# Kernel optimization log

Measured on AMD Instinct MI355X. Metric: run time of the kernel, lower is better.

Reference implementation:

```python
import jax, jax.numpy as jnp
import numpy as np

B, N, H = 32, 2048, 512
MASK_NEG = 1e30  # matches torch mask_logic constant


def setup_inputs() -> dict:
    key = jax.random.key(0)
    ks = jax.random.split(key, 10)
    Q = jax.random.normal(ks[0], (B, H), dtype=jnp.float32)
    K = jax.random.normal(ks[1], (B, N, H), dtype=jnp.float32)
    V = jax.random.normal(ks[2], (B, N, H), dtype=jnp.float32)
    adj = jax.random.randint(ks[3], (B, N), 0, 2, dtype=jnp.int32)
    s_mask = jax.random.randint(ks[4], (B, N), 0, 2, dtype=jnp.int32)
    s = 1.0 / np.sqrt(H)
    w_att = jax.random.uniform(ks[5], (1, 2 * H), jnp.float32, -s, s)  # nn.Linear(2H,1) weight
    b_att = jax.random.uniform(ks[6], (1,), jnp.float32, -s, s)
    Wr0 = jax.random.uniform(ks[7], (H, H), jnp.float32, -s, s)
    Wr1 = jax.random.uniform(ks[8], (H, H), jnp.float32, -s, s)
    Wri = jax.random.uniform(ks[9], (H, H), jnp.float32, -s, s)
    return {"Q": Q, "K": K, "V": V, "adj": adj, "s_mask": s_mask,
            "w_att": w_att, "b_att": b_att, "Wr0": Wr0, "Wr1": Wr1, "Wri": Wri}


def reference(Q, K, V, adj, s_mask, w_att, b_att, Wr0, Wr1, Wri):
    Hdim = Q.shape[-1]
    # additive score: linear(cat(Q_exp, K)) split into Q-part + K-part (avoids materializing [B,N,2H])
    wq, wk = w_att[:, :Hdim], w_att[:, Hdim:]          # [1,H] each
    alpha = (Q @ wq[0]) [:, None] + K @ wk[0] + b_att[0]  # [B,N]
    # adjacency mask + softmax over neighbors
    masked = alpha - (1.0 - adj.astype(jnp.float32)) * MASK_NEG
    attn = jax.nn.softmax(masked, axis=1)               # [B,N]
    # gated value projection: V0 where s_mask==1, V1 where 0
    V0 = jnp.einsum('bnh,oh->bno', V, Wr0)
    V1 = jnp.einsum('bnh,oh->bno', V, Wr1)
    sm = s_mask.astype(jnp.float32)[..., None]          # [B,N,1]
    Vm = V0 * sm + V1 * (1.0 - sm)
    # weighted aggregation + residual projection
    attn_sum = jnp.einsum('bn,bnh->bh', attn, Vm) + Q @ Wri.T
    return attn[:, None, :], attn_sum                   # ([B,1,N], [B,H])
```

## Files before the change

kernel.cpp:

```cpp
#include <hip/hip_runtime.h>

#define BB 32
#define NN 2048
#define HH 512
#define MASK_NEG 1e30f

static __device__ __forceinline__ float dot4(float4 a, float4 b) {
    return a.x * b.x + a.y * b.y + a.z * b.z + a.w * b.w;
}

__global__ void k_scores(const float* __restrict__ K,
                         const float* __restrict__ w_att,
                         const int* __restrict__ adj,
                         float* __restrict__ scores) {
    int wave = (blockIdx.x * blockDim.x + threadIdx.x) >> 6;
    int lane = threadIdx.x & 63;
    if (wave >= BB * NN) return;
    const float* wk = w_att + HH;
    size_t base = (size_t)wave * HH;
    float4 k0 = *(const float4*)(K + base + lane * 4);
    float4 k1 = *(const float4*)(K + base + 256 + lane * 4);
    float4 a0 = *(const float4*)(wk + lane * 4);
    float4 a1 = *(const float4*)(wk + 256 + lane * 4);
    float s = dot4(k0, a0) + dot4(k1, a1);
#pragma unroll
    for (int off = 32; off > 0; off >>= 1) s += __shfl_down(s, off, 64);
    if (lane == 0) scores[wave] = adj[wave] ? s : -MASK_NEG;
}

__global__ void k_softmax(float* __restrict__ attn) {
    __shared__ float red[4];
    int b = blockIdx.x;
    int t = threadIdx.x;
    float v[8];
    float m = -INFINITY;
#pragma unroll
    for (int i = 0; i < 8; i++) {
        v[i] = attn[b * NN + t * 8 + i];
        m = fmaxf(m, v[i]);
    }
#pragma unroll
    for (int off = 32; off > 0; off >>= 1) m = fmaxf(m, __shfl_xor(m, off, 64));
    if ((t & 63) == 0) red[t >> 6] = m;
    __syncthreads();
    float m4 = fmaxf(fmaxf(red[0], red[1]), fmaxf(red[2], red[3]));
    float sum = 0.0f;
#pragma unroll
    for (int i = 0; i < 8; i++) {
        v[i] = expf(v[i] - m4);
        sum += v[i];
    }
#pragma unroll
    for (int off = 32; off > 0; off >>= 1) sum += __shfl_xor(sum, off, 64);
    __syncthreads();
    if ((t & 63) == 0) red[t >> 6] = sum;
    __syncthreads();
    float inv = 1.0f / (red[0] + red[1] + red[2] + red[3]);
#pragma unroll
    for (int i = 0; i < 8; i++) attn[b * NN + t * 8 + i] = v[i] * inv;
}

__global__ void k_wsum(const float* __restrict__ V,
                       const float* __restrict__ attn,
                       const int* __restrict__ s_mask,
                       float* __restrict__ u0,
                       float* __restrict__ u1) {
    int b = blockIdx.x >> 4;
    int chunk = blockIdx.x & 15;
    int n0 = chunk * 128;
    int t = threadIdx.x;
    int h4 = (t & 127) * 4;
    int half = t >> 7;
    __shared__ float w0s[128], w1s[128];
    if (t < 128) {
        float w = attn[b * NN + n0 + t];
        int sm = s_mask[b * NN + n0 + t];
        w0s[t] = sm ? w : 0.0f;
        w1s[t] = sm ? 0.0f : w;
    }
    __syncthreads();
    float4 a0 = {0, 0, 0, 0}, a1 = {0, 0, 0, 0};
    const float* Vb = V + ((size_t)(b * NN + n0 + half * 64)) * HH + h4;
#pragma unroll 4
    for (int i = 0; i < 64; i++) {
        float4 x = *(const float4*)(Vb + (size_t)i * HH);
        float w0 = w0s[half * 64 + i];
        float w1 = w1s[half * 64 + i];
        a0.x += w0 * x.x; a0.y += w0 * x.y; a0.z += w0 * x.z; a0.w += w0 * x.w;
        a1.x += w1 * x.x; a1.y += w1 * x.y; a1.z += w1 * x.z; a1.w += w1 * x.w;
    }
    float* p0 = u0 + b * HH + h4;
    float* p1 = u1 + b * HH + h4;
    atomicAdd(p0 + 0, a0.x); atomicAdd(p0 + 1, a0.y);
    atomicAdd(p0 + 2, a0.z); atomicAdd(p0 + 3, a0.w);
    atomicAdd(p1 + 0, a1.x); atomicAdd(p1 + 1, a1.y);
    atomicAdd(p1 + 2, a1.z); atomicAdd(p1 + 3, a1.w);
}

__global__ void k_out(const float* __restrict__ Q,
                      const float* __restrict__ Wr0,
                      const float* __restrict__ Wr1,
                      const float* __restrict__ Wri,
                      const float* __restrict__ u0,
                      const float* __restrict__ u1,
                      float* __restrict__ out) {
    int wave = (blockIdx.x * blockDim.x + threadIdx.x) >> 6;
    int lane = threadIdx.x & 63;
    if (wave >= BB * HH) return;
    int b = wave >> 9;
    int o = wave & 511;
    const float* q = Q + b * HH;
    const float* a = u0 + b * HH;
    const float* c = u1 + b * HH;
    const float* r0 = Wr0 + (size_t)o * HH;
    const float* r1 = Wr1 + (size_t)o * HH;
    const float* ri = Wri + (size_t)o * HH;
    float s = 0.0f;
#pragma unroll
    for (int part = 0; part < 2; part++) {
        int h = part * 256 + lane * 4;
        s += dot4(*(const float4*)(r0 + h), *(const float4*)(a + h));
        s += dot4(*(const float4*)(r1 + h), *(const float4*)(c + h));
        s += dot4(*(const float4*)(ri + h), *(const float4*)(q + h));
    }
#pragma unroll
    for (int off = 32; off > 0; off >>= 1) s += __shfl_down(s, off, 64);
    if (lane == 0) out[wave] = s;
}

extern "C" void kernel_launch(void* const* d_in, const int* in_sizes, int n_in,
                              void* d_out, int out_size, void* d_ws, size_t ws_size,
                              hipStream_t stream) {
    const float* Q = (const float*)d_in[0];
    const float* K = (const float*)d_in[1];
    const float* V = (const float*)d_in[2];
    const int* adj = (const int*)d_in[3];
    const int* s_mask = (const int*)d_in[4];
    const float* w_att = (const float*)d_in[5];
    const float* Wr0 = (const float*)d_in[7];
    const float* Wr1 = (const float*)d_in[8];
    const float* Wri = (const float*)d_in[9];

    float* out = (float*)d_out;
    float* attn = out;
    float* attn_sum = out + BB * NN;
    float* u0 = (float*)d_ws;
    float* u1 = u0 + BB * HH;

    hipMemsetAsync(d_ws, 0, 2 * BB * HH * sizeof(float), stream);
    k_scores<<<(BB * NN) / 4, 256, 0, stream>>>(K, w_att, adj, attn);
    k_softmax<<<BB, 256, 0, stream>>>(attn);
    k_wsum<<<BB * 16, 256, 0, stream>>>(V, attn, s_mask, u0, u1);
    k_out<<<(BB * HH) / 4, 256, 0, stream>>>(Q, Wr0, Wr1, Wri, u0, u1, attn_sum);
}
```

Baseline: 312.1 us.

## Fuse all stages into one cooperative kernel with grid-wide syncs

Replaces the memset plus four kernel launches with a single cooperative kernel of 512 blocks that zeroes the workspace, then computes scores, softmax, the masked weighted sum of V and the output projection, separated by grid.sync. Each wave now handles 32 score rows and 8 output units. The two halves of a block are combined in shared memory before the atomics, which halves atomic traffic. This removes launch gaps and per-kernel tails, but the softmax phase runs on only 32 blocks while the rest wait, and each grid sync adds latency.

```diff
diff --git a/kernel.cpp b/kernel.cpp
--- a/kernel.cpp
+++ b/kernel.cpp
@@ -1,131 +1,162 @@
 #include <hip/hip_runtime.h>
+#include <hip/hip_cooperative_groups.h>
+
+namespace cg = cooperative_groups;
 
 #define BB 32
 #define NN 2048
 #define HH 512
-#define MASK_NEG 1e30f
 
 static __device__ __forceinline__ float dot4(float4 a, float4 b) {
     return a.x * b.x + a.y * b.y + a.z * b.z + a.w * b.w;
 }
 
-__global__ void k_scores(const float* __restrict__ K,
-                         const float* __restrict__ w_att,
-                         const int* __restrict__ adj,
-                         float* __restrict__ scores) {
-    int wave = (blockIdx.x * blockDim.x + threadIdx.x) >> 6;
-    int lane = threadIdx.x & 63;
-    if (wave >= BB * NN) return;
-    const float* wk = w_att + HH;
-    size_t base = (size_t)wave * HH;
-    float4 k0 = *(const float4*)(K + base + lane * 4);
-    float4 k1 = *(const float4*)(K + base + 256 + lane * 4);
-    float4 a0 = *(const float4*)(wk + lane * 4);
-    float4 a1 = *(const float4*)(wk + 256 + lane * 4);
-    float s = dot4(k0, a0) + dot4(k1, a1);
+static __device__ __forceinline__ float waveRedSum(float s) {
 #pragma unroll
     for (int off = 32; off > 0; off >>= 1) s += __shfl_down(s, off, 64);
-    if (lane == 0) scores[wave] = adj[wave] ? s : -MASK_NEG;
+    return s;
 }
 
-__global__ void k_softmax(float* __restrict__ attn) {
-    __shared__ float red[4];
-    int b = blockIdx.x;
+__global__ void __launch_bounds__(256, 2)
+k_fused(const float* __restrict__ Q, const float* __restrict__ K,
+        const float* __restrict__ V, const int* __restrict__ adj,
+        const int* __restrict__ s_mask, const float* __restrict__ w_att,
+        const float* __restrict__ Wr0, const float* __restrict__ Wr1,
+        const float* __restrict__ Wri, float* __restrict__ out,
+        float* __restrict__ ws) {
+    cg::grid_group grid = cg::this_grid();
+    float* attn = out;
+    float* attn_sum = out + BB * NN;
+    float* u0 = ws;
+    float* u1 = ws + BB * HH;
+
+    __shared__ float smem[1280];
+
     int t = threadIdx.x;
-    float v[8];
-    float m = -INFINITY;
+    int blk = blockIdx.x;
+    int gtid = blk * 256 + t;
+    int wave = gtid >> 6;
+    int lane = t & 63;
+
+    if (gtid < 2 * BB * HH) ws[gtid] = 0.0f;
+
+    {
+        const float* wk = w_att + HH;
+        float4 a0 = *(const float4*)(wk + lane * 4);
+        float4 a1 = *(const float4*)(wk + 256 + lane * 4);
+#pragma unroll 4
+        for (int i = 0; i < 32; i++) {
+            int r = wave * 32 + i;
+            size_t base = (size_t)r * HH;
+            float4 k0 = *(const float4*)(K + base + lane * 4);
+            float4 k1 = *(const float4*)(K + base + 256 + lane * 4);
+            float s = waveRedSum(dot4(k0, a0) + dot4(k1, a1));
+            if (lane == 0) attn[r] = adj[r] ? s : -1e30f;
+        }
+    }
+    grid.sync();
+
+    if (blk < BB) {
+        float* red = smem;
+        int b = blk;
+        float v[8];
+        float m = -INFINITY;
 #pragma unroll
-    for (int i = 0; i < 8; i++) {
-        v[i] = attn[b * NN + t * 8 + i];
-        m = fmaxf(m, v[i]);
+        for (int i = 0; i < 8; i++) {
+            v[i] = attn[b * NN + t * 8 + i];
+            m = fmaxf(m, v[i]);
+        }
+#pragma unroll
+        for (int off = 32; off > 0; off >>= 1) m = fmaxf(m, __shfl_xor(m, off, 64));
+        if (lane == 0) red[t >> 6] = m;
+        __syncthreads();
+        float m4 = fmaxf(fmaxf(red[0], red[1]), fmaxf(red[2], red[3]));
+        float sum = 0.0f;
+#pragma unroll
+        for (int i = 0; i < 8; i++) {
+            v[i] = expf(v[i] - m4);
+            sum += v[i];
+        }
+#pragma unroll
+        for (int off = 32; off > 0; off >>= 1) sum += __shfl_xor(sum, off, 64);
+        __syncthreads();
+        if (lane == 0) red[t >> 6] = sum;
+        __syncthreads();
+        float inv = 1.0f / (red[0] + red[1] + red[2] + red[3]);
+#pragma unroll
+        for (int i = 0; i < 8; i++) attn[b * NN + t * 8 + i] = v[i] * inv;
     }
+    grid.sync();
+
+    {
+        float* w0s = smem;
+        float* w1s = smem + 128;
+        float* comb = smem + 256;
+        int b = blk >> 4;
+        int n0 = (blk & 15) * 128;
+        int h4 = (t & 127) * 4;
+        int half = t >> 7;
+        if (t < 128) {
+            float w = attn[b * NN + n0 + t];
+            int sm = s_mask[b * NN + n0 + t];
+            w0s[t] = sm ? w : 0.0f;
+            w1s[t] = sm ? 0.0f : w;
+        }
+        __syncthreads();
+        float4 a0 = {0, 0, 0, 0}, a1 = {0, 0, 0, 0};
+        const float* Vb = V + ((size_t)(b * NN + n0 + half * 64)) * HH + h4;
+#pragma unroll 4
+        for (int i = 0; i < 64; i++) {
+            float4 x = *(const float4*)(Vb + (size_t)i * HH);
+            float w0 = w0s[half * 64 + i];
+            float w1 = w1s[half * 64 + i];
+            a0.x += w0 * x.x; a0.y += w0 * x.y; a0.z += w0 * x.z; a0.w += w0 * x.w;
+            a1.x += w1 * x.x; a1.y += w1 * x.y; a1.z += w1 * x.z; a1.w += w1 * x.w;
+        }
+        if (half == 1) {
+            int i8 = (t - 128) * 8;
+            comb[i8 + 0] = a0.x; comb[i8 + 1] = a0.y; comb[i8 + 2] = a0.z; comb[i8 + 3] = a0.w;
+            comb[i8 + 4] = a1.x; comb[i8 + 5] = a1.y; comb[i8 + 6] = a1.z; comb[i8 + 7] = a1.w;
+        }
+        __syncthreads();
+        if (half == 0) {
+            int i8 = t * 8;
+            a0.x += comb[i8 + 0]; a0.y += comb[i8 + 1]; a0.z += comb[i8 + 2]; a0.w += comb[i8 + 3];
+            a1.x += comb[i8 + 4]; a1.y += comb[i8 + 5]; a1.z += comb[i8 + 6]; a1.w += comb[i8 + 7];
+            float* p0 = u0 + b * HH + h4;
+            float* p1 = u1 + b * HH + h4;
+            atomicAdd(p0 + 0, a0.x); atomicAdd(p0 + 1, a0.y);
+            atomicAdd(p0 + 2, a0.z); atomicAdd(p0 + 3, a0.w);
+            atomicAdd(p1 + 0, a1.x); atomicAdd(p1 + 1, a1.y);
+            atomicAdd(p1 + 2, a1.z); atomicAdd(p1 + 3, a1.w);
+        }
+    }
+    grid.sync();
+
+    {
 #pragma unroll
-    for (int off = 32; off > 0; off >>= 1) m = fmaxf(m, __shfl_xor(m, off, 64));
-    if ((t & 63) == 0) red[t >> 6] = m;
-    __syncthreads();
-    float m4 = fmaxf(fmaxf(red[0], red[1]), fmaxf(red[2], red[3]));
-    float sum = 0.0f;
+        for (int i = 0; i < 8; i++) {
+            int unit = wave * 8 + i;
+            int b = unit >> 9;
+            int o = unit & 511;
+            const float* q = Q + b * HH;
+            const float* x0 = u0 + b * HH;
+            const float* x1 = u1 + b * HH;
+            const float* r0 = Wr0 + (size_t)o * HH;
+            const float* r1 = Wr1 + (size_t)o * HH;
+            const float* ri = Wri + (size_t)o * HH;
+            float s = 0.0f;
 #pragma unroll
-    for (int i = 0; i < 8; i++) {
-        v[i] = expf(v[i] - m4);
-        sum += v[i];
+            for (int part = 0; part < 2; part++) {
+                int h = part * 256 + lane * 4;
+                s += dot4(*(const float4*)(r0 + h), *(const float4*)(x0 + h));
+                s += dot4(*(const float4*)(r1 + h), *(const float4*)(x1 + h));
+                s += dot4(*(const float4*)(ri + h), *(const float4*)(q + h));
+            }
+            s = waveRedSum(s);
+            if (lane == 0) attn_sum[unit] = s;
+        }
     }
-#pragma unroll
-    for (int off = 32; off > 0; off >>= 1) sum += __shfl_xor(sum, off, 64);
-    __syncthreads();
-    if ((t & 63) == 0) red[t >> 6] = sum;
-    __syncthreads();
-    float inv = 1.0f / (red[0] + red[1] + red[2] + red[3]);
-#pragma unroll
-    for (int i = 0; i < 8; i++) attn[b * NN + t * 8 + i] = v[i] * inv;
-}
-
-__global__ void k_wsum(const float* __restrict__ V,
-                       const float* __restrict__ attn,
-                       const int* __restrict__ s_mask,
-                       float* __restrict__ u0,
-                       float* __restrict__ u1) {
-    int b = blockIdx.x >> 4;
-    int chunk = blockIdx.x & 15;
-    int n0 = chunk * 128;
-    int t = threadIdx.x;
-    int h4 = (t & 127) * 4;
-    int half = t >> 7;
-    __shared__ float w0s[128], w1s[128];
-    if (t < 128) {
-        float w = attn[b * NN + n0 + t];
-        int sm = s_mask[b * NN + n0 + t];
-        w0s[t] = sm ? w : 0.0f;
-        w1s[t] = sm ? 0.0f : w;
-    }
-    __syncthreads();
-    float4 a0 = {0, 0, 0, 0}, a1 = {0, 0, 0, 0};
-    const float* Vb = V + ((size_t)(b * NN + n0 + half * 64)) * HH + h4;
-#pragma unroll 4
-    for (int i = 0; i < 64; i++) {
-        float4 x = *(const float4*)(Vb + (size_t)i * HH);
-        float w0 = w0s[half * 64 + i];
-        float w1 = w1s[half * 64 + i];
-        a0.x += w0 * x.x; a0.y += w0 * x.y; a0.z += w0 * x.z; a0.w += w0 * x.w;
-        a1.x += w1 * x.x; a1.y += w1 * x.y; a1.z += w1 * x.z; a1.w += w1 * x.w;
-    }
-    float* p0 = u0 + b * HH + h4;
-    float* p1 = u1 + b * HH + h4;
-    atomicAdd(p0 + 0, a0.x); atomicAdd(p0 + 1, a0.y);
-    atomicAdd(p0 + 2, a0.z); atomicAdd(p0 + 3, a0.w);
-    atomicAdd(p1 + 0, a1.x); atomicAdd(p1 + 1, a1.y);
-    atomicAdd(p1 + 2, a1.z); atomicAdd(p1 + 3, a1.w);
-}
-
-__global__ void k_out(const float* __restrict__ Q,
-                      const float* __restrict__ Wr0,
-                      const float* __restrict__ Wr1,
-                      const float* __restrict__ Wri,
-                      const float* __restrict__ u0,
-                      const float* __restrict__ u1,
-                      float* __restrict__ out) {
-    int wave = (blockIdx.x * blockDim.x + threadIdx.x) >> 6;
-    int lane = threadIdx.x & 63;
-    if (wave >= BB * HH) return;
-    int b = wave >> 9;
-    int o = wave & 511;
-    const float* q = Q + b * HH;
-    const float* a = u0 + b * HH;
-    const float* c = u1 + b * HH;
-    const float* r0 = Wr0 + (size_t)o * HH;
-    const float* r1 = Wr1 + (size_t)o * HH;
-    const float* ri = Wri + (size_t)o * HH;
-    float s = 0.0f;
-#pragma unroll
-    for (int part = 0; part < 2; part++) {
-        int h = part * 256 + lane * 4;
-        s += dot4(*(const float4*)(r0 + h), *(const float4*)(a + h));
-        s += dot4(*(const float4*)(r1 + h), *(const float4*)(c + h));
-        s += dot4(*(const float4*)(ri + h), *(const float4*)(q + h));
-    }
-#pragma unroll
-    for (int off = 32; off > 0; off >>= 1) s += __shfl_down(s, off, 64);
-    if (lane == 0) out[wave] = s;
 }
 
 extern "C" void kernel_launch(void* const* d_in, const int* in_sizes, int n_in,
@@ -140,16 +171,9 @@
     const float* Wr0 = (const float*)d_in[7];
     const float* Wr1 = (const float*)d_in[8];
     const float* Wri = (const float*)d_in[9];
+    float* out = (float*)d_out;
+    float* ws = (float*)d_ws;
 
-    float* out = (float*)d_out;
-    float* attn = out;
-    float* attn_sum = out + BB * NN;
-    float* u0 = (float*)d_ws;
-    float* u1 = u0 + BB * HH;
-
-    hipMemsetAsync(d_ws, 0, 2 * BB * HH * sizeof(float), stream);
-    k_scores<<<(BB * NN) / 4, 256, 0, stream>>>(K, w_att, adj, attn);
-    k_softmax<<<BB, 256, 0, stream>>>(attn);
-    k_wsum<<<BB * 16, 256, 0, stream>>>(V, attn, s_mask, u0, u1);
-    k_out<<<(BB * HH) / 4, 256, 0, stream>>>(Q, Wr0, Wr1, Wri, u0, u1, attn_sum);
+    void* args[] = {&Q, &K, &V, &adj, &s_mask, &w_att, &Wr0, &Wr1, &Wri, &out, &ws};
+    hipLaunchCooperativeKernel((void*)k_fused, dim3(512), dim3(256), args, 0, stream);
 }
```

After: 510.1 us. +63.4%, slower.

## Fold memset into score kernel, defer softmax normalization, combine halves before atomics

Applied to the files above, without the earlier changes.

Zeroing of the accumulation workspace moves into the score kernel, which removes the separate memset launch. The softmax kernel now only computes per-row max and inverse sum, and the weighted-sum kernel applies exp and normalization while writing the attention output, so the normalized probabilities no longer take an extra read-write pass. Inside the weighted-sum kernel the two half-blocks are summed through shared memory before the atomic adds, which halves global atomic traffic at the cost of an extra barrier and 4KB of shared memory.

```diff
diff --git a/kernel.cpp b/kernel.cpp
--- a/kernel.cpp
+++ b/kernel.cpp
@@ -3,17 +3,20 @@
 #define BB 32
 #define NN 2048
 #define HH 512
-#define MASK_NEG 1e30f
 
 static __device__ __forceinline__ float dot4(float4 a, float4 b) {
     return a.x * b.x + a.y * b.y + a.z * b.z + a.w * b.w;
 }
 
+
 __global__ void k_scores(const float* __restrict__ K,
                          const float* __restrict__ w_att,
                          const int* __restrict__ adj,
-                         float* __restrict__ scores) {
-    int wave = (blockIdx.x * blockDim.x + threadIdx.x) >> 6;
+                         float* __restrict__ scores,
+                         float* __restrict__ ws) {
+    int gtid = blockIdx.x * blockDim.x + threadIdx.x;
+    if (gtid < 2 * BB * HH) ws[gtid] = 0.0f;
+    int wave = gtid >> 6;
     int lane = threadIdx.x & 63;
     if (wave >= BB * NN) return;
     const float* wk = w_att + HH;
@@ -25,10 +28,11 @@
     float s = dot4(k0, a0) + dot4(k1, a1);
 #pragma unroll
     for (int off = 32; off > 0; off >>= 1) s += __shfl_down(s, off, 64);
-    if (lane == 0) scores[wave] = adj[wave] ? s : -MASK_NEG;
+    if (lane == 0) scores[wave] = adj[wave] ? s : -1e30f;
 }
 
-__global__ void k_softmax(float* __restrict__ attn) {
+__global__ void k_rowstats(const float* __restrict__ scores,
+                           float* __restrict__ stats) {
     __shared__ float red[4];
     int b = blockIdx.x;
     int t = threadIdx.x;
@@ -36,7 +40,7 @@
     float m = -INFINITY;
 #pragma unroll
     for (int i = 0; i < 8; i++) {
-        v[i] = attn[b * NN + t * 8 + i];
+        v[i] = scores[b * NN + t * 8 + i];
         m = fmaxf(m, v[i]);
     }
 #pragma unroll
@@ -46,34 +50,35 @@
     float m4 = fmaxf(fmaxf(red[0], red[1]), fmaxf(red[2], red[3]));
     float sum = 0.0f;
 #pragma unroll
-    for (int i = 0; i < 8; i++) {
-        v[i] = expf(v[i] - m4);
-        sum += v[i];
-    }
+    for (int i = 0; i < 8; i++) sum += expf(v[i] - m4);
 #pragma unroll
     for (int off = 32; off > 0; off >>= 1) sum += __shfl_xor(sum, off, 64);
     __syncthreads();
     if ((t & 63) == 0) red[t >> 6] = sum;
     __syncthreads();
-    float inv = 1.0f / (red[0] + red[1] + red[2] + red[3]);
-#pragma unroll
-    for (int i = 0; i < 8; i++) attn[b * NN + t * 8 + i] = v[i] * inv;
+    if (t == 0) {
+        stats[b] = m4;
+        stats[32 + b] = 1.0f / (red[0] + red[1] + red[2] + red[3]);
+    }
 }
 
 __global__ void k_wsum(const float* __restrict__ V,
-                       const float* __restrict__ attn,
+                       float* __restrict__ attn,
                        const int* __restrict__ s_mask,
+                       const float* __restrict__ stats,
                        float* __restrict__ u0,
                        float* __restrict__ u1) {
     int b = blockIdx.x >> 4;
-    int chunk = blockIdx.x & 15;
-    int n0 = chunk * 128;
+    int n0 = (blockIdx.x & 15) * 128;
     int t = threadIdx.x;
     int h4 = (t & 127) * 4;
     int half = t >> 7;
-    __shared__ float w0s[128], w1s[128];
+    __shared__ float w0s[128], w1s[128], comb[1024];
     if (t < 128) {
-        float w = attn[b * NN + n0 + t];
+        float mb = stats[b];
+        float invb = stats[32 + b];
+        float w = expf(attn[b * NN + n0 + t] - mb) * invb;
+        attn[b * NN + n0 + t] = w;
         int sm = s_mask[b * NN + n0 + t];
         w0s[t] = sm ? w : 0.0f;
         w1s[t] = sm ? 0.0f : w;
@@ -89,12 +94,23 @@
         a0.x += w0 * x.x; a0.y += w0 * x.y; a0.z += w0 * x.z; a0.w += w0 * x.w;
         a1.x += w1 * x.x; a1.y += w1 * x.y; a1.z += w1 * x.z; a1.w += w1 * x.w;
     }
-    float* p0 = u0 + b * HH + h4;
-    float* p1 = u1 + b * HH + h4;
-    atomicAdd(p0 + 0, a0.x); atomicAdd(p0 + 1, a0.y);
-    atomicAdd(p0 + 2, a0.z); atomicAdd(p0 + 3, a0.w);
-    atomicAdd(p1 + 0, a1.x); atomicAdd(p1 + 1, a1.y);
-    atomicAdd(p1 + 2, a1.z); atomicAdd(p1 + 3, a1.w);
+    if (half == 1) {
+        int i8 = (t - 128) * 8;
+        comb[i8 + 0] = a0.x; comb[i8 + 1] = a0.y; comb[i8 + 2] = a0.z; comb[i8 + 3] = a0.w;
+        comb[i8 + 4] = a1.x; comb[i8 + 5] = a1.y; comb[i8 + 6] = a1.z; comb[i8 + 7] = a1.w;
+    }
+    __syncthreads();
+    if (half == 0) {
+        int i8 = t * 8;
+        a0.x += comb[i8 + 0]; a0.y += comb[i8 + 1]; a0.z += comb[i8 + 2]; a0.w += comb[i8 + 3];
+        a1.x += comb[i8 + 4]; a1.y += comb[i8 + 5]; a1.z += comb[i8 + 6]; a1.w += comb[i8 + 7];
+        float* p0 = u0 + b * HH + h4;
+        float* p1 = u1 + b * HH + h4;
+        atomicAdd(p0 + 0, a0.x); atomicAdd(p0 + 1, a0.y);
+        atomicAdd(p0 + 2, a0.z); atomicAdd(p0 + 3, a0.w);
+        atomicAdd(p1 + 0, a1.x); atomicAdd(p1 + 1, a1.y);
+        atomicAdd(p1 + 2, a1.z); atomicAdd(p1 + 3, a1.w);
+    }
 }
 
 __global__ void k_out(const float* __restrict__ Q,
@@ -110,8 +126,8 @@
     int b = wave >> 9;
     int o = wave & 511;
     const float* q = Q + b * HH;
-    const float* a = u0 + b * HH;
-    const float* c = u1 + b * HH;
+    const float* x0 = u0 + b * HH;
+    const float* x1 = u1 + b * HH;
     const float* r0 = Wr0 + (size_t)o * HH;
     const float* r1 = Wr1 + (size_t)o * HH;
     const float* ri = Wri + (size_t)o * HH;
@@ -119,8 +135,8 @@
 #pragma unroll
     for (int part = 0; part < 2; part++) {
         int h = part * 256 + lane * 4;
-        s += dot4(*(const float4*)(r0 + h), *(const float4*)(a + h));
-        s += dot4(*(const float4*)(r1 + h), *(const float4*)(c + h));
+        s += dot4(*(const float4*)(r0 + h), *(const float4*)(x0 + h));
+        s += dot4(*(const float4*)(r1 + h), *(const float4*)(x1 + h));
         s += dot4(*(const float4*)(ri + h), *(const float4*)(q + h));
     }
 #pragma unroll
@@ -144,12 +160,13 @@
     float* out = (float*)d_out;
     float* attn = out;
     float* attn_sum = out + BB * NN;
-    float* u0 = (float*)d_ws;
-    float* u1 = u0 + BB * HH;
+    float* ws = (float*)d_ws;
+    float* u0 = ws;
+    float* u1 = ws + BB * HH;
+    float* stats = ws + 2 * BB * HH;
 
-    hipMemsetAsync(d_ws, 0, 2 * BB * HH * sizeof(float), stream);
-    k_scores<<<(BB * NN) / 4, 256, 0, stream>>>(K, w_att, adj, attn);
-    k_softmax<<<BB, 256, 0, stream>>>(attn);
-    k_wsum<<<BB * 16, 256, 0, stream>>>(V, attn, s_mask, u0, u1);
+    k_scores<<<(BB * NN) / 4, 256, 0, stream>>>(K, w_att, adj, attn, ws);
+    k_rowstats<<<BB, 256, 0, stream>>>(attn, stats);
+    k_wsum<<<BB * 16, 256, 0, stream>>>(V, attn, s_mask, stats, u0, u1);
     k_out<<<(BB * HH) / 4, 256, 0, stream>>>(Q, Wr0, Wr1, Wri, u0, u1, attn_sum);
 }
```

After: 304.1 us. 1.03x faster.
